# Kernel optimization log

Measured on AMD Instinct MI355X. Metric: run time of the kernel, lower is better.

## Reference

```python
import jax, jax.numpy as jnp
import numpy as np

CAPACITY_FACTOR = 1.25

def setup_inputs() -> dict:
    key = jax.random.key(0)
    k0, k1, k2, k3 = jax.random.split(key, 4)
    B, S, D, E = 2, 4096, 1024, 8
    H = 4 * D
    x = jax.random.normal(k0, (B, S, D), dtype=jnp.float32)
    # router: nn.Linear(d_model, num_experts, bias=False), init std=0.01, weight shape [E, D]
    router_w = jax.random.normal(k1, (E, D), dtype=jnp.float32) * 0.01
    W1 = jax.random.normal(k2, (E, D, H), dtype=jnp.float32) * (1.0 / np.sqrt(D))
    b1 = jnp.zeros((E, H), dtype=jnp.float32)
    W2 = jax.random.normal(k3, (E, H, D), dtype=jnp.float32) * (1.0 / np.sqrt(H))
    b2 = jnp.zeros((E, D), dtype=jnp.float32)
    return {"x": x, "router_w": router_w, "W1": W1, "b1": b1, "W2": W2, "b2": b2}


def reference(x, router_w, W1, b1, W2, b2):
    # Eval-mode Switch Transformer MoE: top-1 routing, capacity drop, no dropout,
    # load_balancing_loss = 0 (self.training is False).
    B, S, D = x.shape
    E = router_w.shape[0]
    T = B * S
    CAP = int(CAPACITY_FACTOR * T / E)  # expert_capacity

    xf = x.reshape(T, D)
    logits = xf @ router_w.T                      # [T, E]
    probs = jax.nn.softmax(logits, axis=-1)       # [T, E]
    gate = jnp.max(probs, axis=-1)                # [T]
    eidx = jnp.argmax(probs, axis=-1)             # [T] top-1 expert per token

    # Rank tokens within each expert by gate descending (== torch.topk capacity keep).
    order = jnp.lexsort((-gate, eidx))            # primary: expert, secondary: gate desc
    se = eidx[order]                              # sorted expert ids
    start = jnp.searchsorted(se, jnp.arange(E))   # first position of each expert group
    pos_sorted = jnp.arange(T) - start[se]        # rank within group
    pos = jnp.zeros(T, dtype=jnp.int32).at[order].set(pos_sorted.astype(jnp.int32))
    keep = pos < CAP                              # tokens over capacity are dropped (output 0)
    pos_c = jnp.where(keep, pos, 0)

    # Dispatch into [E, CAP, D] buffer; dropped tokens contribute zeros at slot 0.
    buf = jnp.zeros((E, CAP, D), dtype=x.dtype).at[eidx, pos_c].add(xf * keep[:, None])

    # Per-expert dense MLP (grouped GEMM): Linear -> ReLU -> Linear.
    h = jax.nn.relu(jnp.einsum('ecd,edh->ech', buf, W1) + b1[:, None, :])
    ob = jnp.einsum('ech,ehd->ecd', h, W2) + b2[:, None, :]

    # Combine: gather back, scale by top-1 gate, zero out dropped tokens.
    y = ob[eidx, pos_c] * (gate * keep)[:, None]
    out = y.reshape(B, S, D)

    router_entropy = -jnp.sum(probs * jnp.log(probs + 1e-8), axis=-1).mean()
    assignment_counts = jnp.zeros(E, dtype=x.dtype).at[eidx].add(1.0)
    return out, router_entropy, assignment_counts
```

## Files before the change

### kernel.cpp

```cpp
#include <hip/hip_runtime.h>
#include <stdint.h>

#define T_TOK 8192
#define D_DIM 1024
#define E_NUM 8
#define H_DIM 4096
#define CAPQ  1280
#define CAPR  1280
#define MT_MAX 10

typedef __bf16 bf16x8 __attribute__((ext_vector_type(8)));
typedef float  f32x4  __attribute__((ext_vector_type(4)));
typedef const __attribute__((address_space(1))) void glb_void;
typedef __attribute__((address_space(3))) void lds_void;

__device__ __forceinline__ unsigned short f2bf(float f) {
  union { float f; unsigned u; } v; v.f = f;
  return (unsigned short)((v.u + 0x7FFFu + ((v.u >> 16) & 1u)) >> 16);
}

__global__ __launch_bounds__(256) void router_kernel(
    const float* __restrict__ x, const float* __restrict__ rw,
    float* __restrict__ gate, int* __restrict__ eidx,
    int* __restrict__ cnt, float* __restrict__ entacc)
{
  __shared__ float wl[E_NUM * D_DIM];
  __shared__ float sent[4];
  const int tid = threadIdx.x;
  for (int i = tid; i < E_NUM * D_DIM / 4; i += 256)
    ((float4*)wl)[i] = ((const float4*)rw)[i];
  __syncthreads();

  const int wid = tid >> 6, lane = tid & 63;
  const int t = blockIdx.x * 4 + wid;
  float acc[E_NUM];
#pragma unroll
  for (int e = 0; e < E_NUM; ++e) acc[e] = 0.f;
  const float* xr = x + (size_t)t * D_DIM;
  for (int k = 0; k < D_DIM / 64; ++k) {
    float xv = xr[k * 64 + lane];
#pragma unroll
    for (int e = 0; e < E_NUM; ++e) acc[e] += xv * wl[e * D_DIM + k * 64 + lane];
  }
#pragma unroll
  for (int e = 0; e < E_NUM; ++e) {
#pragma unroll
    for (int off = 32; off; off >>= 1) acc[e] += __shfl_xor(acc[e], off);
  }
  float entv = 0.f;
  if (lane == 0) {
    float mx = acc[0]; int am = 0;
#pragma unroll
    for (int e = 1; e < E_NUM; ++e) if (acc[e] > mx) { mx = acc[e]; am = e; }
    float p[E_NUM], s = 0.f;
#pragma unroll
    for (int e = 0; e < E_NUM; ++e) { p[e] = __expf(acc[e] - mx); s += p[e]; }
    const float inv = 1.f / s;
    float g = 0.f, ent = 0.f;
#pragma unroll
    for (int e = 0; e < E_NUM; ++e) {
      float pe = p[e] * inv;
      ent -= pe * __logf(pe + 1e-8f);
      if (e == am) g = pe;
    }
    gate[t] = g;
    eidx[t] = am;
    atomicAdd(&cnt[am], 1);
    entv = ent * (1.0f / T_TOK);
  }
  if (lane == 0) sent[wid] = entv;
  __syncthreads();
  if (tid == 0) atomicAdd(entacc, sent[0] + sent[1] + sent[2] + sent[3]);
}

__global__ __launch_bounds__(256) void dispatch_kernel(
    const float* __restrict__ x, const int* __restrict__ eidx,
    int* __restrict__ cursor, int* __restrict__ perm,
    unsigned short* __restrict__ xs)
{
  const int tid = threadIdx.x, wid = tid >> 6, lane = tid & 63;
  const int t = blockIdx.x * 4 + wid;
  const int e = eidx[t];
  int slot = 0;
  if (lane == 0) slot = atomicAdd(&cursor[e], 1);
  slot = __shfl(slot, 0);
  if (slot >= CAPQ) return;
  if (lane == 0) perm[e * CAPR + slot] = t;
  const float4* xr = (const float4*)(x + (size_t)t * D_DIM);
  unsigned short* dst = xs + ((size_t)e * CAPR + slot) * D_DIM;
#pragma unroll
  for (int i = 0; i < 4; ++i) {
    float4 v = xr[i * 64 + lane];
    ushort4 o;
    o.x = f2bf(v.x); o.y = f2bf(v.y); o.z = f2bf(v.z); o.w = f2bf(v.w);
    ((ushort4*)dst)[i * 64 + lane] = o;
  }
}

template<int R, int C>
__global__ __launch_bounds__(256) void transpose_conv(
    const float* __restrict__ src, unsigned short* __restrict__ dst)
{
  __shared__ float tl[32][33];
  const int e = blockIdx.z;
  const float* s = src + (size_t)e * R * C;
  unsigned short* d = dst + (size_t)e * R * C;
  const int tx = threadIdx.x, ty = threadIdx.y;
  const int c0 = blockIdx.x * 32, r0 = blockIdx.y * 32;
#pragma unroll
  for (int i = 0; i < 4; ++i)
    tl[ty + i * 8][tx] = s[(size_t)(r0 + ty + i * 8) * C + c0 + tx];
  __syncthreads();
#pragma unroll
  for (int i = 0; i < 4; ++i)
    d[(size_t)(c0 + ty + i * 8) * R + r0 + tx] = f2bf(tl[tx][ty + i * 8]);
}

template<int K, int N, int EPI>
__global__ __launch_bounds__(256, 2) void gemm_moe(
    const unsigned short* __restrict__ A,
    const unsigned short* __restrict__ Bt,
    const float* __restrict__ bias,
    const int* __restrict__ cnt,
    unsigned short* __restrict__ hout,
    float* __restrict__ out,
    const int* __restrict__ perm,
    const float* __restrict__ gate)
{
  __shared__ __align__(16) unsigned short As[2][128 * 64];
  __shared__ __align__(16) unsigned short Bs[2][128 * 64];

  const int e = blockIdx.z;
  int c = cnt[e]; if (c > CAPQ) c = CAPQ;
  const int row0 = blockIdx.y * 128;
  if (row0 >= c) return;
  const int n0 = blockIdx.x * 128;

  const int tid = threadIdx.x;
  const int wid = tid >> 6, lane = tid & 63;
  const int wm = wid >> 1, wn = wid & 1;
  const int srow = wid * 32 + (lane >> 3);
  const int sk = (lane & 7) * 8;
  const int fr = lane & 15, fk = (lane >> 4) * 8;

  const unsigned short* Abase = A + ((size_t)e * CAPR + row0) * K;
  const unsigned short* Bbase = Bt + ((size_t)e * N + n0) * K;

  f32x4 acc[4][4];
#pragma unroll
  for (int m = 0; m < 4; ++m)
#pragma unroll
    for (int n = 0; n < 4; ++n) acc[m][n] = f32x4{0.f, 0.f, 0.f, 0.f};

#pragma unroll
  for (int i = 0; i < 4; ++i) {
    __builtin_amdgcn_global_load_lds(
        (glb_void*)(Abase + (size_t)(srow + i * 8) * K + sk),
        (lds_void*)(&As[0][wid * 2048 + i * 512]), 16, 0, 0);
    __builtin_amdgcn_global_load_lds(
        (glb_void*)(Bbase + (size_t)(srow + i * 8) * K + sk),
        (lds_void*)(&Bs[0][wid * 2048 + i * 512]), 16, 0, 0);
  }
  asm volatile("s_waitcnt vmcnt(0)" ::: "memory");
  __syncthreads();

  int cur = 0;
  const int NT = K / 64;
  for (int t = 0; t < NT; ++t) {
    if (t + 1 < NT) {
      const int ko = (t + 1) * 64;
#pragma unroll
      for (int i = 0; i < 4; ++i) {
        __builtin_amdgcn_global_load_lds(
            (glb_void*)(Abase + (size_t)(srow + i * 8) * K + ko + sk),
            (lds_void*)(&As[cur ^ 1][wid * 2048 + i * 512]), 16, 0, 0);
        __builtin_amdgcn_global_load_lds(
            (glb_void*)(Bbase + (size_t)(srow + i * 8) * K + ko + sk),
            (lds_void*)(&Bs[cur ^ 1][wid * 2048 + i * 512]), 16, 0, 0);
      }
    }
    const unsigned short* Ap = As[cur];
    const unsigned short* Bp = Bs[cur];
#pragma unroll
    for (int kk = 0; kk < 2; ++kk) {
      bf16x8 af[4], bfm[4];
#pragma unroll
      for (int m = 0; m < 4; ++m)
        af[m] = *(const bf16x8*)(Ap + ((wm * 64 + m * 16 + fr) * 64 + kk * 32 + fk));
#pragma unroll
      for (int n = 0; n < 4; ++n)
        bfm[n] = *(const bf16x8*)(Bp + ((wn * 64 + n * 16 + fr) * 64 + kk * 32 + fk));
#pragma unroll
      for (int m = 0; m < 4; ++m)
#pragma unroll
        for (int n = 0; n < 4; ++n)
          acc[m][n] = __builtin_amdgcn_mfma_f32_16x16x32_bf16(af[m], bfm[n], acc[m][n], 0, 0, 0);
    }
    asm volatile("s_waitcnt vmcnt(0)" ::: "memory");
    __syncthreads();
    cur ^= 1;
  }

  const int frow = (lane >> 4) * 4;
  const int fcol = lane & 15;
#pragma unroll
  for (int m = 0; m < 4; ++m) {
#pragma unroll
    for (int n = 0; n < 4; ++n) {
      const int col = n0 + wn * 64 + n * 16 + fcol;
      const float bv = bias[e * N + col];
      if (EPI == 0) {
#pragma unroll
        for (int j = 0; j < 4; ++j) {
          const int r = wm * 64 + m * 16 + frow + j;
          float v = acc[m][n][j] + bv;
          v = v > 0.f ? v : 0.f;
          hout[((size_t)e * CAPR + row0 + r) * N + col] = f2bf(v);
        }
      } else {
#pragma unroll
        for (int j = 0; j < 4; ++j) {
          const int r = row0 + wm * 64 + m * 16 + frow + j;
          const int tok = perm[e * CAPR + r];
          if (tok >= 0)
            out[(size_t)tok * N + col] = (acc[m][n][j] + bv) * gate[tok];
        }
      }
    }
  }
}

__global__ void finalize_kernel(const float* __restrict__ entacc,
                                const int* __restrict__ cnt,
                                float* __restrict__ tail)
{
  const int i = threadIdx.x;
  if (i == 0) tail[0] = *entacc;
  if (i < E_NUM) tail[1 + i] = (float)cnt[i];
}

extern "C" void kernel_launch(void* const* d_in, const int* in_sizes, int n_in,
                              void* d_out, int out_size, void* d_ws, size_t ws_size,
                              hipStream_t stream) {
  const float* x  = (const float*)d_in[0];
  const float* rw = (const float*)d_in[1];
  const float* W1 = (const float*)d_in[2];
  const float* b1 = (const float*)d_in[3];
  const float* W2 = (const float*)d_in[4];
  const float* b2 = (const float*)d_in[5];
  float* out = (float*)d_out;

  char* ws = (char*)d_ws;
  size_t off = 0;
  auto alloc = [&](size_t bytes) -> void* {
    void* p = ws + off;
    off = (off + bytes + 255) & ~(size_t)255;
    return p;
  };
  unsigned short* WT   = (unsigned short*)alloc((size_t)E_NUM * D_DIM * H_DIM * 2);
  unsigned short* xs   = (unsigned short*)alloc((size_t)E_NUM * CAPR * D_DIM * 2);
  unsigned short* h    = (unsigned short*)alloc((size_t)E_NUM * CAPR * H_DIM * 2);
  float* gate   = (float*)alloc(T_TOK * 4);
  int*   eidx   = (int*)alloc(T_TOK * 4);
  int*   perm   = (int*)alloc(E_NUM * CAPR * 4);
  int*   cnt    = (int*)alloc(256);
  int*   cursor = (int*)alloc(256);
  float* entacc = (float*)alloc(256);

  hipMemsetAsync(d_out, 0, (size_t)out_size * 4, stream);
  hipMemsetAsync(xs, 0, (size_t)E_NUM * CAPR * D_DIM * 2, stream);
  hipMemsetAsync(perm, 0xFF, E_NUM * CAPR * 4, stream);
  hipMemsetAsync(cnt, 0, 256, stream);
  hipMemsetAsync(cursor, 0, 256, stream);
  hipMemsetAsync(entacc, 0, 256, stream);

  router_kernel<<<T_TOK / 4, 256, 0, stream>>>(x, rw, gate, eidx, cnt, entacc);
  dispatch_kernel<<<T_TOK / 4, 256, 0, stream>>>(x, eidx, cursor, perm, xs);

  transpose_conv<D_DIM, H_DIM><<<dim3(H_DIM / 32, D_DIM / 32, E_NUM), dim3(32, 8), 0, stream>>>(W1, WT);
  gemm_moe<D_DIM, H_DIM, 0><<<dim3(H_DIM / 128, MT_MAX, E_NUM), 256, 0, stream>>>(
      xs, WT, b1, cnt, h, nullptr, nullptr, nullptr);

  transpose_conv<H_DIM, D_DIM><<<dim3(D_DIM / 32, H_DIM / 32, E_NUM), dim3(32, 8), 0, stream>>>(W2, WT);
  gemm_moe<H_DIM, D_DIM, 1><<<dim3(D_DIM / 128, MT_MAX, E_NUM), 256, 0, stream>>>(
      h, WT, b2, cnt, nullptr, out, perm, gate);

  finalize_kernel<<<1, 64, 0, stream>>>(entacc, cnt, out + (size_t)T_TOK * D_DIM);
}
```

Baseline: 953.9 us.

## Fuse router with dispatch, widen weight transpose, single-buffer GEMM for occupancy

Merges the router and dispatch kernels so each token's row is read once and its bf16 copy is scattered using the slot returned by the counting atomic. This removes the separate eidx and cursor buffers and one launch. The weight transpose moves to 64x64 tiles with float4 loads and 16-byte bf16 stores to raise memory efficiency. The GEMM drops LDS double buffering and raises launch bounds to 5 blocks per CU, trading load/compute overlap within a block for more resident blocks. Slot order within an expert is now arrival order, as before, so capacity dropping still differs from the reference's gate-ranked order.

```diff
diff --git a/kernel.cpp b/kernel.cpp
--- a/kernel.cpp
+++ b/kernel.cpp
@@ -11,6 +11,8 @@
 
 typedef __bf16 bf16x8 __attribute__((ext_vector_type(8)));
 typedef float  f32x4  __attribute__((ext_vector_type(4)));
+typedef unsigned short u16x8 __attribute__((ext_vector_type(8)));
+typedef unsigned short u16x4 __attribute__((ext_vector_type(4)));
 typedef const __attribute__((address_space(1))) void glb_void;
 typedef __attribute__((address_space(3))) void lds_void;
 
@@ -19,10 +21,10 @@
   return (unsigned short)((v.u + 0x7FFFu + ((v.u >> 16) & 1u)) >> 16);
 }
 
-__global__ __launch_bounds__(256) void router_kernel(
+__global__ __launch_bounds__(256) void router_dispatch_kernel(
     const float* __restrict__ x, const float* __restrict__ rw,
-    float* __restrict__ gate, int* __restrict__ eidx,
-    int* __restrict__ cnt, float* __restrict__ entacc)
+    float* __restrict__ gate, int* __restrict__ cnt, float* __restrict__ entacc,
+    int* __restrict__ perm, unsigned short* __restrict__ xs)
 {
   __shared__ float wl[E_NUM * D_DIM];
   __shared__ float sent[4];
@@ -33,23 +35,29 @@
 
   const int wid = tid >> 6, lane = tid & 63;
   const int t = blockIdx.x * 4 + wid;
+  const float4* xr = (const float4*)(x + (size_t)t * D_DIM);
+  float4 xv[4];
   float acc[E_NUM];
 #pragma unroll
   for (int e = 0; e < E_NUM; ++e) acc[e] = 0.f;
-  const float* xr = x + (size_t)t * D_DIM;
-  for (int k = 0; k < D_DIM / 64; ++k) {
-    float xv = xr[k * 64 + lane];
-#pragma unroll
-    for (int e = 0; e < E_NUM; ++e) acc[e] += xv * wl[e * D_DIM + k * 64 + lane];
+#pragma unroll
+  for (int k = 0; k < 4; ++k) {
+    xv[k] = xr[k * 64 + lane];
+#pragma unroll
+    for (int e = 0; e < E_NUM; ++e) {
+      float4 w = ((const float4*)wl)[e * 256 + k * 64 + lane];
+      acc[e] += xv[k].x * w.x + xv[k].y * w.y + xv[k].z * w.z + xv[k].w * w.w;
+    }
   }
 #pragma unroll
   for (int e = 0; e < E_NUM; ++e) {
 #pragma unroll
     for (int off = 32; off; off >>= 1) acc[e] += __shfl_xor(acc[e], off);
   }
+  int am = 0, slot = 0;
   float entv = 0.f;
   if (lane == 0) {
-    float mx = acc[0]; int am = 0;
+    float mx = acc[0];
 #pragma unroll
     for (int e = 1; e < E_NUM; ++e) if (acc[e] > mx) { mx = acc[e]; am = e; }
     float p[E_NUM], s = 0.f;
@@ -64,60 +72,58 @@
       if (e == am) g = pe;
     }
     gate[t] = g;
-    eidx[t] = am;
-    atomicAdd(&cnt[am], 1);
+    slot = atomicAdd(&cnt[am], 1);
     entv = ent * (1.0f / T_TOK);
+  }
+  am = __shfl(am, 0);
+  slot = __shfl(slot, 0);
+  if (slot < CAPQ) {
+    if (lane == 0) perm[am * CAPR + slot] = t;
+    unsigned short* dst = xs + ((size_t)am * CAPR + slot) * D_DIM;
+#pragma unroll
+    for (int k = 0; k < 4; ++k) {
+      u16x4 o;
+      o[0] = f2bf(xv[k].x); o[1] = f2bf(xv[k].y);
+      o[2] = f2bf(xv[k].z); o[3] = f2bf(xv[k].w);
+      *(u16x4*)(dst + k * 256 + lane * 4) = o;
+    }
   }
   if (lane == 0) sent[wid] = entv;
   __syncthreads();
   if (tid == 0) atomicAdd(entacc, sent[0] + sent[1] + sent[2] + sent[3]);
 }
 
-__global__ __launch_bounds__(256) void dispatch_kernel(
-    const float* __restrict__ x, const int* __restrict__ eidx,
-    int* __restrict__ cursor, int* __restrict__ perm,
-    unsigned short* __restrict__ xs)
-{
-  const int tid = threadIdx.x, wid = tid >> 6, lane = tid & 63;
-  const int t = blockIdx.x * 4 + wid;
-  const int e = eidx[t];
-  int slot = 0;
-  if (lane == 0) slot = atomicAdd(&cursor[e], 1);
-  slot = __shfl(slot, 0);
-  if (slot >= CAPQ) return;
-  if (lane == 0) perm[e * CAPR + slot] = t;
-  const float4* xr = (const float4*)(x + (size_t)t * D_DIM);
-  unsigned short* dst = xs + ((size_t)e * CAPR + slot) * D_DIM;
-#pragma unroll
-  for (int i = 0; i < 4; ++i) {
-    float4 v = xr[i * 64 + lane];
-    ushort4 o;
-    o.x = f2bf(v.x); o.y = f2bf(v.y); o.z = f2bf(v.z); o.w = f2bf(v.w);
-    ((ushort4*)dst)[i * 64 + lane] = o;
-  }
-}
-
 template<int R, int C>
 __global__ __launch_bounds__(256) void transpose_conv(
     const float* __restrict__ src, unsigned short* __restrict__ dst)
 {
-  __shared__ float tl[32][33];
+  __shared__ float tl[64][65];
   const int e = blockIdx.z;
   const float* s = src + (size_t)e * R * C;
   unsigned short* d = dst + (size_t)e * R * C;
-  const int tx = threadIdx.x, ty = threadIdx.y;
-  const int c0 = blockIdx.x * 32, r0 = blockIdx.y * 32;
-#pragma unroll
-  for (int i = 0; i < 4; ++i)
-    tl[ty + i * 8][tx] = s[(size_t)(r0 + ty + i * 8) * C + c0 + tx];
+  const int tid = threadIdx.x;
+  const int c0 = blockIdx.x * 64, r0 = blockIdx.y * 64;
+  const int lr = tid >> 4, lc = (tid & 15) * 4;
+#pragma unroll
+  for (int i = 0; i < 4; ++i) {
+    float4 v = *(const float4*)(s + (size_t)(r0 + lr + i * 16) * C + c0 + lc);
+    tl[lr + i * 16][lc + 0] = v.x; tl[lr + i * 16][lc + 1] = v.y;
+    tl[lr + i * 16][lc + 2] = v.z; tl[lr + i * 16][lc + 3] = v.w;
+  }
   __syncthreads();
-#pragma unroll
-  for (int i = 0; i < 4; ++i)
-    d[(size_t)(c0 + ty + i * 8) * R + r0 + tx] = f2bf(tl[tx][ty + i * 8]);
+  const int oc = tid >> 3, orr = (tid & 7) * 8;
+#pragma unroll
+  for (int p = 0; p < 2; ++p) {
+    const int cc = oc + p * 32;
+    u16x8 o;
+#pragma unroll
+    for (int j = 0; j < 8; ++j) o[j] = f2bf(tl[orr + j][cc]);
+    *(u16x8*)(d + (size_t)(c0 + cc) * R + r0 + orr) = o;
+  }
 }
 
 template<int K, int N, int EPI>
-__global__ __launch_bounds__(256, 2) void gemm_moe(
+__global__ __launch_bounds__(256, 5) void gemm_moe(
     const unsigned short* __restrict__ A,
     const unsigned short* __restrict__ Bt,
     const float* __restrict__ bias,
@@ -127,8 +133,8 @@
     const int* __restrict__ perm,
     const float* __restrict__ gate)
 {
-  __shared__ __align__(16) unsigned short As[2][128 * 64];
-  __shared__ __align__(16) unsigned short Bs[2][128 * 64];
+  __shared__ __align__(16) unsigned short As[128 * 64];
+  __shared__ __align__(16) unsigned short Bs[128 * 64];
 
   const int e = blockIdx.z;
   int c = cnt[e]; if (c > CAPQ) c = CAPQ;
@@ -152,53 +158,36 @@
 #pragma unroll
     for (int n = 0; n < 4; ++n) acc[m][n] = f32x4{0.f, 0.f, 0.f, 0.f};
 
-#pragma unroll
-  for (int i = 0; i < 4; ++i) {
-    __builtin_amdgcn_global_load_lds(
-        (glb_void*)(Abase + (size_t)(srow + i * 8) * K + sk),
-        (lds_void*)(&As[0][wid * 2048 + i * 512]), 16, 0, 0);
-    __builtin_amdgcn_global_load_lds(
-        (glb_void*)(Bbase + (size_t)(srow + i * 8) * K + sk),
-        (lds_void*)(&Bs[0][wid * 2048 + i * 512]), 16, 0, 0);
-  }
-  asm volatile("s_waitcnt vmcnt(0)" ::: "memory");
-  __syncthreads();
-
-  int cur = 0;
   const int NT = K / 64;
   for (int t = 0; t < NT; ++t) {
-    if (t + 1 < NT) {
-      const int ko = (t + 1) * 64;
-#pragma unroll
-      for (int i = 0; i < 4; ++i) {
-        __builtin_amdgcn_global_load_lds(
-            (glb_void*)(Abase + (size_t)(srow + i * 8) * K + ko + sk),
-            (lds_void*)(&As[cur ^ 1][wid * 2048 + i * 512]), 16, 0, 0);
-        __builtin_amdgcn_global_load_lds(
-            (glb_void*)(Bbase + (size_t)(srow + i * 8) * K + ko + sk),
-            (lds_void*)(&Bs[cur ^ 1][wid * 2048 + i * 512]), 16, 0, 0);
-      }
-    }
-    const unsigned short* Ap = As[cur];
-    const unsigned short* Bp = Bs[cur];
+    const int ko = t * 64;
+#pragma unroll
+    for (int i = 0; i < 4; ++i) {
+      __builtin_amdgcn_global_load_lds(
+          (glb_void*)(Abase + (size_t)(srow + i * 8) * K + ko + sk),
+          (lds_void*)(&As[wid * 2048 + i * 512]), 16, 0, 0);
+      __builtin_amdgcn_global_load_lds(
+          (glb_void*)(Bbase + (size_t)(srow + i * 8) * K + ko + sk),
+          (lds_void*)(&Bs[wid * 2048 + i * 512]), 16, 0, 0);
+    }
+    asm volatile("s_waitcnt vmcnt(0)" ::: "memory");
+    __syncthreads();
 #pragma unroll
     for (int kk = 0; kk < 2; ++kk) {
       bf16x8 af[4], bfm[4];
 #pragma unroll
       for (int m = 0; m < 4; ++m)
-        af[m] = *(const bf16x8*)(Ap + ((wm * 64 + m * 16 + fr) * 64 + kk * 32 + fk));
+        af[m] = *(const bf16x8*)(As + ((wm * 64 + m * 16 + fr) * 64 + kk * 32 + fk));
 #pragma unroll
       for (int n = 0; n < 4; ++n)
-        bfm[n] = *(const bf16x8*)(Bp + ((wn * 64 + n * 16 + fr) * 64 + kk * 32 + fk));
+        bfm[n] = *(const bf16x8*)(Bs + ((wn * 64 + n * 16 + fr) * 64 + kk * 32 + fk));
 #pragma unroll
       for (int m = 0; m < 4; ++m)
 #pragma unroll
         for (int n = 0; n < 4; ++n)
           acc[m][n] = __builtin_amdgcn_mfma_f32_16x16x32_bf16(af[m], bfm[n], acc[m][n], 0, 0, 0);
     }
-    asm volatile("s_waitcnt vmcnt(0)" ::: "memory");
     __syncthreads();
-    cur ^= 1;
   }
 
   const int frow = (lane >> 4) * 4;
@@ -261,27 +250,23 @@
   unsigned short* xs   = (unsigned short*)alloc((size_t)E_NUM * CAPR * D_DIM * 2);
   unsigned short* h    = (unsigned short*)alloc((size_t)E_NUM * CAPR * H_DIM * 2);
   float* gate   = (float*)alloc(T_TOK * 4);
-  int*   eidx   = (int*)alloc(T_TOK * 4);
   int*   perm   = (int*)alloc(E_NUM * CAPR * 4);
   int*   cnt    = (int*)alloc(256);
-  int*   cursor = (int*)alloc(256);
   float* entacc = (float*)alloc(256);
 
   hipMemsetAsync(d_out, 0, (size_t)out_size * 4, stream);
   hipMemsetAsync(xs, 0, (size_t)E_NUM * CAPR * D_DIM * 2, stream);
   hipMemsetAsync(perm, 0xFF, E_NUM * CAPR * 4, stream);
   hipMemsetAsync(cnt, 0, 256, stream);
-  hipMemsetAsync(cursor, 0, 256, stream);
   hipMemsetAsync(entacc, 0, 256, stream);
 
-  router_kernel<<<T_TOK / 4, 256, 0, stream>>>(x, rw, gate, eidx, cnt, entacc);
-  dispatch_kernel<<<T_TOK / 4, 256, 0, stream>>>(x, eidx, cursor, perm, xs);
-
-  transpose_conv<D_DIM, H_DIM><<<dim3(H_DIM / 32, D_DIM / 32, E_NUM), dim3(32, 8), 0, stream>>>(W1, WT);
+  router_dispatch_kernel<<<T_TOK / 4, 256, 0, stream>>>(x, rw, gate, cnt, entacc, perm, xs);
+
+  transpose_conv<D_DIM, H_DIM><<<dim3(H_DIM / 64, D_DIM / 64, E_NUM), 256, 0, stream>>>(W1, WT);
   gemm_moe<D_DIM, H_DIM, 0><<<dim3(H_DIM / 128, MT_MAX, E_NUM), 256, 0, stream>>>(
       xs, WT, b1, cnt, h, nullptr, nullptr, nullptr);
 
-  transpose_conv<H_DIM, D_DIM><<<dim3(D_DIM / 32, H_DIM / 32, E_NUM), dim3(32, 8), 0, stream>>>(W2, WT);
+  transpose_conv<H_DIM, D_DIM><<<dim3(D_DIM / 64, H_DIM / 64, E_NUM), 256, 0, stream>>>(W2, WT);
   gemm_moe<H_DIM, D_DIM, 1><<<dim3(D_DIM / 128, MT_MAX, E_NUM), 256, 0, stream>>>(
       h, WT, b2, cnt, nullptr, out, perm, gate);
 
```

Result: faster. 848.0 us (-11.1%).
